# Optimization experiments

Measured on AMD Instinct MI355X. Metric: run time of the kernel, lower is better.

The kernel has to match this reference:

```python
import jax, jax.numpy as jnp
import numpy as np

NUM_HEADS = 16
HEAD_DIM = 64
MEMORY_SIZE = 65536
K_SIMILAR = 8
K_CONTIGUOUS = 2
SURPRISE_THRESHOLD = 0.5
EPS = 1e-8  # torch F.cosine_similarity eps


def setup_inputs() -> dict:
    key = jax.random.key(0)
    ks = jax.random.split(key, 6)
    B, H, S, HD = 4, NUM_HEADS, 8192, HEAD_DIM
    D = H * HD
    inputs = jax.random.normal(ks[0], (B, S, D), dtype=jnp.float32)
    q = jax.random.normal(ks[1], (B, H, S, HD), dtype=jnp.float32)
    k = jax.random.normal(ks[2], (B, H, S, HD), dtype=jnp.float32)
    v = jax.random.normal(ks[3], (B, H, S, HD), dtype=jnp.float32)
    attention_mask = jnp.ones((B, S), dtype=jnp.float32)
    events = jax.random.normal(ks[4], (MEMORY_SIZE, D), dtype=jnp.float32)
    return {"inputs": inputs, "q": q, "k": k, "v": v,
            "attention_mask": attention_mask, "events": events,
            "seq_len_q": 8192}


def _segment_mean(kf, seg, S):
    # kf: [S, D], seg: [S] int32 segment ids (exclusive cumsum of boundary mask)
    sums = jax.ops.segment_sum(kf, seg, num_segments=S)          # [S, D]
    cnts = jax.ops.segment_sum(jnp.ones_like(seg, jnp.float32), seg, num_segments=S)
    means = sums / jnp.maximum(cnts, 1.0)[:, None]
    return means, cnts


def reference(inputs, q, k, v, attention_mask, events, seq_len_q):
    B, H, S, HD = k.shape
    D = H * HD
    # flatten keys per token: [B, S, H*HD]
    kf = k.transpose(0, 2, 1, 3).reshape(B, S, D)

    # --- surprise scores: ||k_t - k_{t-1}|| padded with 0 at t=0 ---
    diffs = kf[:, 1:] - kf[:, :-1]
    norms = jnp.linalg.norm(diffs, axis=-1)                      # [B, S-1]
    surprise = jnp.pad(norms, ((0, 0), (1, 0)))                  # [B, S]

    # --- event segmentation (threshold = mean + c*std, unbiased std like torch) ---
    mean = jnp.mean(surprise, axis=1, keepdims=True)
    std = jnp.std(surprise, axis=1, ddof=1, keepdims=True)
    bmask = surprise > (mean + SURPRISE_THRESHOLD * std)
    bmask = bmask.at[:, -1].set(True)                            # last index is always a boundary
    bi = bmask.astype(jnp.int32)
    seg = jnp.cumsum(bi, axis=1) - bi                            # token t -> #boundaries before t

    # --- memory update: mean-pool keys within each event (scatter) ---
    new_events, event_lengths = jax.vmap(_segment_mean, in_axes=(0, 0, None))(kf, seg, S)
    # new_events: [B, S, D] (rows >= num_events are zero), event_lengths: [B, S]

    # --- retrieval: cosine sim of last-token key vs memory, top-k gather ---
    query = kf[:, -1]                                            # [B, D]
    qn = jnp.maximum(jnp.linalg.norm(query, axis=-1), EPS)       # [B]
    en = jnp.maximum(jnp.linalg.norm(events, axis=-1), EPS)      # [M]
    sims = (query @ events.T) / (qn[:, None] * en[None, :])      # [B, M]
    kt = min(K_SIMILAR + K_CONTIGUOUS, events.shape[0])
    _, idx = jax.lax.top_k(sims, kt)                             # [B, kt]

    ret = events[idx]                                            # [B, kt, D]
    ret = ret.reshape(B, kt, H, HD).transpose(0, 2, 1, 3)        # [B, H, kt, HD]
    ret_k, ret_v = ret, ret                                      # non-differential: v == k slice

    aug_k = jnp.concatenate([ret_k, k], axis=2)                  # [B, H, kt+S, HD]
    aug_v = jnp.concatenate([ret_v, v], axis=2)
    aug_mask = jnp.concatenate([jnp.ones((B, kt), attention_mask.dtype), attention_mask], axis=1)

    cp = seq_len_q - 1
    ret_pos = jnp.linspace(float(cp - kt), float(cp - 1), kt, dtype=jnp.float32)
    pos = jnp.arange(S, dtype=jnp.float32)
    aug_positions = jnp.broadcast_to(jnp.concatenate([ret_pos, pos]), (B, kt + S))

    return (inputs, q, aug_k, aug_v, aug_mask, aug_positions, new_events, event_lengths)
```

## Files before the change

kernel.cpp:

```cpp
#include <hip/hip_runtime.h>
#include <math.h>

#define BB 4
#define HH 16
#define SS 8192
#define HDD 64
#define DD 1024
#define MEM 65536
#define KT 10
#define AUGROWS (SS + KT)

static const long O0 = 0;
static const long O1 = 33554432;
static const long O2 = 67108864;
static const long O3 = 100704256;
static const long O4 = 134299648;
static const long O5 = 134332456;
static const long O6 = 134365264;
static const long O7 = 167919696;

#define WS_NEED_FUSED 5767168UL

#define N4REG 8388608L

typedef float __attribute__((ext_vector_type(4))) f4v;

static __device__ __forceinline__ void nt_store4(float4* p, float4 v) {
    f4v t; t.x = v.x; t.y = v.y; t.z = v.z; t.w = v.w;
    __builtin_nontemporal_store(t, (f4v*)p);
}
static __device__ __forceinline__ float4 nt_load4(const float4* p) {
    f4v t = __builtin_nontemporal_load((const f4v*)p);
    float4 v; v.x = t.x; v.y = t.y; v.z = t.z; v.w = t.w;
    return v;
}

#define K_BLOCKS 2048
#define SIMS_BLOCKS 4096
__global__ __launch_bounds__(256) void bigfused_kernel(
        const float4* __restrict__ k4, const float4* __restrict__ events4,
        float4* __restrict__ out4, double* __restrict__ partial,
        float* __restrict__ sims, int do_part) {
    __shared__ float4 qls4[BB][256];
    int blk = blockIdx.x;
    int tid = threadIdx.x;
    if (blk < K_BLOCKS) {
        long i = ((long)blk) * 256 + tid;
        const long bstride = (long)K_BLOCKS * 256;
        for (; i < N4REG; i += bstride) {
            long chunk = i >> 17;
            long r = i & 131071;
            float4 cur = k4[i];
            out4[(O2 >> 2) + chunk * 131232L + 160 + r] = cur;
            if (do_part) {
                int s = (int)(r >> 4);
                if (s > 0) {
                    float4 pv = k4[i - 16];
                    double dx = (double)cur.x - (double)pv.x;
                    double dy = (double)cur.y - (double)pv.y;
                    double dz = (double)cur.z - (double)pv.z;
                    double dw = (double)cur.w - (double)pv.w;
                    double acc = dx * dx + dy * dy + dz * dz + dw * dw;
                    acc += __shfl_xor(acc, 1, 64);
                    acc += __shfl_xor(acc, 2, 64);
                    acc += __shfl_xor(acc, 4, 64);
                    acc += __shfl_xor(acc, 8, 64);
                    if ((tid & 15) == 0) {
                        int b = (int)(chunk >> 4);
                        int h = (int)(chunk & 15);
                        partial[((long)b * SS + s) * HH + h] = acc;
                    }
                }
            }
        }
    } else {
        for (int j = tid; j < BB * 256; j += 256) {
            int b = j >> 8;
            int f4i = j & 255;
            qls4[b][f4i] =
                k4[((long)(b * HH + (f4i >> 4)) * SS + (SS - 1)) * 16 + (f4i & 15)];
        }
        __syncthreads();
        int w = tid >> 6;
        int lane = tid & 63;
        long e0 = (long)(blk - K_BLOCKS) * 4 + w;
        for (int rr = 0; rr < 4; ++rr) {
            long e = e0 + (long)rr * (4 * SIMS_BLOCKS);
            const float4* er = events4 + e * 256;
            float en = 0.f, d0 = 0.f, d1 = 0.f, d2 = 0.f, d3 = 0.f;
#pragma unroll
            for (int it = 0; it < 4; ++it) {
                int j4 = lane + it * 64;
                float4 ev = nt_load4(er + j4);
                en += ev.x * ev.x + ev.y * ev.y + ev.z * ev.z + ev.w * ev.w;
                float4 q0 = qls4[0][j4];
                d0 += ev.x * q0.x + ev.y * q0.y + ev.z * q0.z + ev.w * q0.w;
                float4 q1 = qls4[1][j4];
                d1 += ev.x * q1.x + ev.y * q1.y + ev.z * q1.z + ev.w * q1.w;
                float4 q2 = qls4[2][j4];
                d2 += ev.x * q2.x + ev.y * q2.y + ev.z * q2.z + ev.w * q2.w;
                float4 q3 = qls4[3][j4];
                d3 += ev.x * q3.x + ev.y * q3.y + ev.z * q3.z + ev.w * q3.w;
            }
            for (int m = 32; m >= 1; m >>= 1) {
                en += __shfl_xor(en, m, 64);
                d0 += __shfl_xor(d0, m, 64);
                d1 += __shfl_xor(d1, m, 64);
                d2 += __shfl_xor(d2, m, 64);
                d3 += __shfl_xor(d3, m, 64);
            }
            if (lane == 0) {
                float enn = fmaxf(sqrtf(en), 1e-8f);
                sims[0 * (long)MEM + e] = d0 / enn;
                sims[1 * (long)MEM + e] = d1 / enn;
                sims[2 * (long)MEM + e] = d2 / enn;
                sims[3 * (long)MEM + e] = d3 / enn;
            }
        }
    }
}

__global__ __launch_bounds__(256) void surprise_fallback_kernel(
        const float* __restrict__ k, double* __restrict__ surprise) {
    int wid = (int)(((long)blockIdx.x * blockDim.x + threadIdx.x) >> 6);
    int lane = threadIdx.x & 63;
    if (wid >= BB * SS) return;
    int b = wid >> 13;
    int s = wid & (SS - 1);
    double acc = 0.0;
    if (s > 0) {
        const float* kb = k + (long)b * HH * SS * HDD;
        for (int h = 0; h < HH; ++h) {
            long off = ((long)h * SS + s) * HDD + lane;
            double d = (double)kb[off] - (double)kb[off - HDD];
            acc += d * d;
        }
        for (int m = 32; m >= 1; m >>= 1) acc += __shfl_xor(acc, m, 64);
    }
    if (lane == 0) surprise[wid] = (s == 0) ? 0.0 : sqrt(acc);
}

__global__ __launch_bounds__(1024) void postfused_kernel(
        const double* __restrict__ partial, double* __restrict__ surprise,
        int* __restrict__ bpos, int* __restrict__ nseg,
        const float* __restrict__ sims, float* __restrict__ cval,
        int* __restrict__ cidx, int* __restrict__ idxout,
        const float* __restrict__ amask, const void* __restrict__ seqp,
        float* __restrict__ out, int* __restrict__ counters, int fused) {
    __shared__ double sd[1024];
    __shared__ int si[1024];
    __shared__ float lv[256][KT];
    __shared__ int li[256][KT];
    int blk = blockIdx.x;
    int tid = threadIdx.x;

    if (blk < 32) {
        if (fused) {
            int t = blk * 1024 + tid;
            int s = t & (SS - 1);
            double acc = 0.0;
            if (s > 0) {
                const double* row = partial + (long)t * HH;
#pragma unroll
                for (int h = 0; h < HH; ++h) acc += row[h];
            }
            surprise[t] = (s == 0) ? 0.0 : sqrt(acc);
        }
        __threadfence();
        __syncthreads();
        if (tid == 0) atomicAdd(&counters[0], 1);
    } else if (blk < 36) {
        if (tid == 0) {
            while (atomicAdd(&counters[0], 0) < 32) __builtin_amdgcn_s_sleep(8);
        }
        __syncthreads();
        __threadfence();
        int b = blk - 32;
        const double* sp = surprise + (long)b * SS;
        double loc[8];
        double sum = 0.0;
        for (int j = 0; j < 8; ++j) { loc[j] = sp[tid * 8 + j]; sum += loc[j]; }
        sd[tid] = sum;
        __syncthreads();
        for (int off = 512; off >= 1; off >>= 1) {
            if (tid < off) sd[tid] += sd[tid + off];
            __syncthreads();
        }
        double mean = sd[0] / SS;
        __syncthreads();
        double vs = 0.0;
        for (int j = 0; j < 8; ++j) { double d = loc[j] - mean; vs += d * d; }
        sd[tid] = vs;
        __syncthreads();
        for (int off = 512; off >= 1; off >>= 1) {
            if (tid < off) sd[tid] += sd[tid + off];
            __syncthreads();
        }
        double thr = mean + 0.5 * sqrt(sd[0] / (SS - 1));
        __syncthreads();
        int bi[8];
        int cnt = 0;
        for (int j = 0; j < 8; ++j) {
            int s = tid * 8 + j;
            bi[j] = (s == SS - 1) || (loc[j] > thr);
            cnt += bi[j];
        }
        si[tid] = cnt;
        __syncthreads();
        for (int off = 1; off < 1024; off <<= 1) {
            int v = 0;
            if (tid >= off) v = si[tid - off];
            __syncthreads();
            si[tid] += v;
            __syncthreads();
        }
        int run = si[tid] - cnt;
        for (int j = 0; j < 8; ++j) {
            if (bi[j]) { bpos[(long)b * SS + run] = tid * 8 + j; ++run; }
        }
        if (tid == 1023) nseg[b] = si[1023];
    } else if (blk < 100) {
        int g = blk - 36;
        int b = g >> 4;
        int part = g & 15;
        if (tid < 256) {
            const float* sb = sims + (long)b * MEM + part * 4096;
            float val[KT];
            int idx[KT];
#pragma unroll
            for (int p = 0; p < KT; ++p) { val[p] = -INFINITY; idx[p] = 0x7fffffff; }
            for (int it = 0; it < 16; ++it) {
                int e = tid + it * 256;
                float v = sb[e];
                if (v > val[KT - 1]) {
#pragma unroll
                    for (int p = KT - 1; p >= 1; --p) {
                        if (v > val[p - 1]) {
                            val[p] = val[p - 1];
                            idx[p] = idx[p - 1];
                        } else {
                            val[p] = v;
                            idx[p] = e;
                            v = -INFINITY;
                        }
                    }
                    if (v != -INFINITY) { val[0] = v; idx[0] = e; }
                }
            }
#pragma unroll
            for (int p = 0; p < KT; ++p) { lv[tid][p] = val[p]; li[tid][p] = idx[p]; }
        }
        for (int off = 128; off >= 1; off >>= 1) {
            __syncthreads();
            if (tid < off) {
                float a_[KT], b_[KT], m_[KT];
                int ai_[KT], bi_[KT], mi_[KT];
#pragma unroll
                for (int p = 0; p < KT; ++p) {
                    a_[p] = lv[tid][p];
                    ai_[p] = li[tid][p];
                    b_[p] = lv[tid + off][p];
                    bi_[p] = li[tid + off][p];
                }
                int pa = 0, pb = 0;
#pragma unroll
                for (int p = 0; p < KT; ++p) {
                    bool ta = (a_[pa] > b_[pb]) ||
                              (a_[pa] == b_[pb] && ai_[pa] < bi_[pb]);
                    if (ta) { m_[p] = a_[pa]; mi_[p] = ai_[pa]; ++pa; }
                    else    { m_[p] = b_[pb]; mi_[p] = bi_[pb]; ++pb; }
                }
#pragma unroll
                for (int p = 0; p < KT; ++p) { lv[tid][p] = m_[p]; li[tid][p] = mi_[p]; }
            }
        }
        __syncthreads();
        if (tid == 0) {
#pragma unroll
            for (int p = 0; p < KT; ++p) {
                cval[g * KT + p] = lv[0][p];
                cidx[g * KT + p] = part * 4096 + li[0][p];
            }
        }
        __threadfence();
        __syncthreads();
        if (tid == 0) atomicAdd(&counters[1], 1);
    } else if (blk < 104) {
        if (tid == 0) {
            while (atomicAdd(&counters[1], 0) < 64) __builtin_amdgcn_s_sleep(8);
        }
        __syncthreads();
        __threadfence();
        int b = blk - 100;
        float mv = -INFINITY;
        int mi = 0x7fffffff;
        if (tid < 160) { mv = cval[b * 160 + tid]; mi = cidx[b * 160 + tid]; }
        if (tid < 256) { lv[tid][0] = mv; li[tid][0] = mi; }
        __syncthreads();
        if (tid == 0) {
            for (int p = 0; p < KT; ++p) {
                float best = -INFINITY;
                int bi = 0x7fffffff;
                int bslot = 0;
                for (int j = 0; j < 160; ++j) {
                    if (lv[j][0] > best || (lv[j][0] == best && li[j][0] < bi)) {
                        best = lv[j][0];
                        bi = li[j][0];
                        bslot = j;
                    }
                }
                idxout[b * KT + p] = bi;
                lv[bslot][0] = -INFINITY;
                li[bslot][0] = 0x7fffffff;
            }
        }
    } else {
        int iv = ((const int*)seqp)[0];
        int seqlen;
        if (iv > 0 && iv < (1 << 24)) seqlen = iv;
        else seqlen = (int)(((const float*)seqp)[0]);
        int cp = seqlen - 1;
        int n = BB * AUGROWS;
        int i = (blk - 104) * 1024 + tid;
        int stride = 16 * 1024;
        for (; i < n; i += stride) {
            int b = i / AUGROWS;
            int t = i - b * AUGROWS;
            out[O4 + i] = (t < KT) ? 1.0f : amask[(long)b * SS + t - KT];
            out[O5 + i] = (t < KT) ? (float)(cp - KT + t) : (float)(t - KT);
        }
    }
}

__global__ __launch_bounds__(256) void segtail_kernel(
        const float4* __restrict__ out4c, const int* __restrict__ bpos,
        const int* __restrict__ nseg, const float* __restrict__ events,
        const int* __restrict__ idxin, float* __restrict__ out) {
    int blk = blockIdx.x;
    int tid = threadIdx.x;
    float4* ne4 = (float4*)(out + O6);
    if (blk < BB * SS) {
        int b = blk >> 13;
        int j = blk & (SS - 1);
        int ns = nseg[b];
        float4* row = ne4 + ((long)b * SS + j) * 256;
        if (j >= ns) {
            nt_store4(row + tid, make_float4(0.f, 0.f, 0.f, 0.f));
            if (tid == 0) out[O7 + (long)b * SS + j] = 0.0f;
            return;
        }
        int start = (j == 0) ? 0 : bpos[(long)b * SS + j - 1] + 1;
        int end = bpos[(long)b * SS + j];
        const float4* kb = out4c + (O2 >> 2) +
                           ((long)(b * HH + (tid >> 4)) * AUGROWS + KT) * 16 +
                           (tid & 15);
        double a0 = 0.0, a1 = 0.0, a2 = 0.0, a3 = 0.0;
        for (int s = start; s <= end; ++s) {
            float4 x = kb[(long)s * 16];
            a0 += (double)x.x; a1 += (double)x.y; a2 += (double)x.z; a3 += (double)x.w;
        }
        double inv = 1.0 / (double)(end - start + 1);
        nt_store4(row + tid, make_float4((float)(a0 * inv), (float)(a1 * inv),
                                         (float)(a2 * inv), (float)(a3 * inv)));
        if (tid == 0) out[O7 + (long)b * SS + j] = (float)(end - start + 1);
    } else {
        int g = blk - BB * SS;
        int b = g / KT;
        int t = g % KT;
        int ev = idxin[b * KT + t];
        for (int c = 0; c < 4; ++c) {
            int j = tid + c * 256;
            float vv = events[(long)ev * DD + j];
            int h = j >> 6;
            int d = j & 63;
            long dst = (((long)b * HH + h) * AUGROWS + t) * HDD + d;
            out[O2 + dst] = vv;
            out[O3 + dst] = vv;
        }
    }
}

extern "C" void kernel_launch(void* const* d_in, const int* in_sizes, int n_in,
                              void* d_out, int out_size, void* d_ws, size_t ws_size,
                              hipStream_t stream) {
    const float* in_inputs = (const float*)d_in[0];
    const float* in_q = (const float*)d_in[1];
    const float* in_k = (const float*)d_in[2];
    const float* in_v = (const float*)d_in[3];
    const float* in_amask = (const float*)d_in[4];
    const float* in_events = (const float*)d_in[5];
    const void* in_seq = d_in[6];
    float* out = (float*)d_out;

    char* ws = (char*)d_ws;
    double* surprise = (double*)ws;
    float* sims = (float*)(ws + 262144);
    int* bpos = (int*)(ws + 1310720);
    int* nseg = (int*)(ws + 1441792);
    int* idxw = (int*)(ws + 1441824);
    float* cval = (float*)(ws + 1442304);
    int* cidx = (int*)(ws + 1444864);
    int* counters = (int*)(ws + 1447424);
    double* partial = (double*)(ws + 1572864);

    const int fused = (ws_size >= WS_NEED_FUSED) ? 1 : 0;

    hipMemsetAsync(counters, 0, 64, stream);
    hipMemcpyAsync(out + O0, in_inputs, 134217728, hipMemcpyDeviceToDevice,
                   stream);
    hipMemcpyAsync(out + O1, in_q, 134217728, hipMemcpyDeviceToDevice, stream);
    hipMemcpy2DAsync(out + O3 + (long)KT * HDD, (size_t)AUGROWS * HDD * 4,
                     in_v, (size_t)SS * HDD * 4, (size_t)SS * HDD * 4,
                     (size_t)BB * HH, hipMemcpyDeviceToDevice, stream);
    bigfused_kernel<<<K_BLOCKS + SIMS_BLOCKS, 256, 0, stream>>>(
        (const float4*)in_k, (const float4*)in_events, (float4*)out, partial,
        sims, fused);
    if (!fused)
        surprise_fallback_kernel<<<8192, 256, 0, stream>>>(in_k, surprise);
    postfused_kernel<<<120, 1024, 0, stream>>>(
        partial, surprise, bpos, nseg, sims, cval, cidx, idxw, in_amask,
        in_seq, out, counters, fused);
    segtail_kernel<<<BB * SS + BB * KT, 256, 0, stream>>>(
        (const float4*)out, bpos, nseg, in_events, idxw, out);
}
```

Measured before the change: 473.7 us.

## Replace hipMemcpy copies with one fused grid-stride copy kernel; split sims kernel

The three runtime memcpy calls (inputs, q, strided v) are dropped. All four tensor copies (inputs, q, k, v), plus the surprise partials computed from k, now run in a single grid-stride kernel that uses nontemporal loads and stores. The cosine-similarity part that used to share a kernel with the k copy becomes its own kernel and launches first. This removes runtime copy overhead and the serialization between copies, but the sims work no longer overlaps with the k copy inside one launch.

```diff
diff --git a/kernel.cpp b/kernel.cpp
--- a/kernel.cpp
+++ b/kernel.cpp
@@ -35,27 +35,34 @@
     return v;
 }
 
-#define K_BLOCKS 2048
-#define SIMS_BLOCKS 4096
-__global__ __launch_bounds__(256) void bigfused_kernel(
-        const float4* __restrict__ k4, const float4* __restrict__ events4,
-        float4* __restrict__ out4, double* __restrict__ partial,
-        float* __restrict__ sims, int do_part) {
-    __shared__ float4 qls4[BB][256];
-    int blk = blockIdx.x;
-    int tid = threadIdx.x;
-    if (blk < K_BLOCKS) {
-        long i = ((long)blk) * 256 + tid;
-        const long bstride = (long)K_BLOCKS * 256;
-        for (; i < N4REG; i += bstride) {
-            long chunk = i >> 17;
-            long r = i & 131071;
-            float4 cur = k4[i];
+#define CPY_BLOCKS 4096
+__global__ __launch_bounds__(256) void copyall_kernel(
+        const float4* __restrict__ in0, const float4* __restrict__ q,
+        const float4* __restrict__ k4, const float4* __restrict__ v,
+        float4* __restrict__ out4, double* __restrict__ partial, int do_part) {
+    long gtid = (long)blockIdx.x * 256 + threadIdx.x;
+    const long stride = (long)CPY_BLOCKS * 256;
+    for (long i = gtid; i < 4 * N4REG; i += stride) {
+        int region = (int)(i >> 23);
+        long rel = i & (N4REG - 1);
+        if (region == 0) {
+            nt_store4(out4 + (O0 >> 2) + rel, nt_load4(in0 + rel));
+        } else if (region == 1) {
+            nt_store4(out4 + (O1 >> 2) + rel, nt_load4(q + rel));
+        } else if (region == 3) {
+            long chunk = rel >> 17;
+            long r = rel & 131071;
+            nt_store4(out4 + (O3 >> 2) + chunk * 131232L + 160 + r,
+                      nt_load4(v + rel));
+        } else {
+            long chunk = rel >> 17;
+            long r = rel & 131071;
+            float4 cur = k4[rel];
             out4[(O2 >> 2) + chunk * 131232L + 160 + r] = cur;
             if (do_part) {
                 int s = (int)(r >> 4);
                 if (s > 0) {
-                    float4 pv = k4[i - 16];
+                    float4 pv = k4[rel - 16];
                     double dx = (double)cur.x - (double)pv.x;
                     double dy = (double)cur.y - (double)pv.y;
                     double dz = (double)cur.z - (double)pv.z;
@@ -65,7 +72,7 @@
                     acc += __shfl_xor(acc, 2, 64);
                     acc += __shfl_xor(acc, 4, 64);
                     acc += __shfl_xor(acc, 8, 64);
-                    if ((tid & 15) == 0) {
+                    if ((threadIdx.x & 15) == 0) {
                         int b = (int)(chunk >> 4);
                         int h = (int)(chunk & 15);
                         partial[((long)b * SS + s) * HH + h] = acc;
@@ -73,49 +80,57 @@
                 }
             }
         }
-    } else {
-        for (int j = tid; j < BB * 256; j += 256) {
-            int b = j >> 8;
-            int f4i = j & 255;
-            qls4[b][f4i] =
-                k4[((long)(b * HH + (f4i >> 4)) * SS + (SS - 1)) * 16 + (f4i & 15)];
-        }
-        __syncthreads();
-        int w = tid >> 6;
-        int lane = tid & 63;
-        long e0 = (long)(blk - K_BLOCKS) * 4 + w;
-        for (int rr = 0; rr < 4; ++rr) {
-            long e = e0 + (long)rr * (4 * SIMS_BLOCKS);
-            const float4* er = events4 + e * 256;
-            float en = 0.f, d0 = 0.f, d1 = 0.f, d2 = 0.f, d3 = 0.f;
-#pragma unroll
-            for (int it = 0; it < 4; ++it) {
-                int j4 = lane + it * 64;
-                float4 ev = nt_load4(er + j4);
-                en += ev.x * ev.x + ev.y * ev.y + ev.z * ev.z + ev.w * ev.w;
-                float4 q0 = qls4[0][j4];
-                d0 += ev.x * q0.x + ev.y * q0.y + ev.z * q0.z + ev.w * q0.w;
-                float4 q1 = qls4[1][j4];
-                d1 += ev.x * q1.x + ev.y * q1.y + ev.z * q1.z + ev.w * q1.w;
-                float4 q2 = qls4[2][j4];
-                d2 += ev.x * q2.x + ev.y * q2.y + ev.z * q2.z + ev.w * q2.w;
-                float4 q3 = qls4[3][j4];
-                d3 += ev.x * q3.x + ev.y * q3.y + ev.z * q3.z + ev.w * q3.w;
-            }
-            for (int m = 32; m >= 1; m >>= 1) {
-                en += __shfl_xor(en, m, 64);
-                d0 += __shfl_xor(d0, m, 64);
-                d1 += __shfl_xor(d1, m, 64);
-                d2 += __shfl_xor(d2, m, 64);
-                d3 += __shfl_xor(d3, m, 64);
-            }
-            if (lane == 0) {
-                float enn = fmaxf(sqrtf(en), 1e-8f);
-                sims[0 * (long)MEM + e] = d0 / enn;
-                sims[1 * (long)MEM + e] = d1 / enn;
-                sims[2 * (long)MEM + e] = d2 / enn;
-                sims[3 * (long)MEM + e] = d3 / enn;
-            }
+    }
+}
+
+#define SIMS_BLOCKS 4096
+__global__ __launch_bounds__(256) void sims_kernel(
+        const float4* __restrict__ k4, const float4* __restrict__ events4,
+        float* __restrict__ sims) {
+    __shared__ float4 qls4[BB][256];
+    int blk = blockIdx.x;
+    int tid = threadIdx.x;
+    for (int j = tid; j < BB * 256; j += 256) {
+        int b = j >> 8;
+        int f4i = j & 255;
+        qls4[b][f4i] =
+            k4[((long)(b * HH + (f4i >> 4)) * SS + (SS - 1)) * 16 + (f4i & 15)];
+    }
+    __syncthreads();
+    int w = tid >> 6;
+    int lane = tid & 63;
+    long e0 = (long)blk * 4 + w;
+    for (int rr = 0; rr < 4; ++rr) {
+        long e = e0 + (long)rr * (4 * SIMS_BLOCKS);
+        const float4* er = events4 + e * 256;
+        float en = 0.f, d0 = 0.f, d1 = 0.f, d2 = 0.f, d3 = 0.f;
+#pragma unroll
+        for (int it = 0; it < 4; ++it) {
+            int j4 = lane + it * 64;
+            float4 ev = nt_load4(er + j4);
+            en += ev.x * ev.x + ev.y * ev.y + ev.z * ev.z + ev.w * ev.w;
+            float4 q0 = qls4[0][j4];
+            d0 += ev.x * q0.x + ev.y * q0.y + ev.z * q0.z + ev.w * q0.w;
+            float4 q1 = qls4[1][j4];
+            d1 += ev.x * q1.x + ev.y * q1.y + ev.z * q1.z + ev.w * q1.w;
+            float4 q2 = qls4[2][j4];
+            d2 += ev.x * q2.x + ev.y * q2.y + ev.z * q2.z + ev.w * q2.w;
+            float4 q3 = qls4[3][j4];
+            d3 += ev.x * q3.x + ev.y * q3.y + ev.z * q3.z + ev.w * q3.w;
+        }
+        for (int m = 32; m >= 1; m >>= 1) {
+            en += __shfl_xor(en, m, 64);
+            d0 += __shfl_xor(d0, m, 64);
+            d1 += __shfl_xor(d1, m, 64);
+            d2 += __shfl_xor(d2, m, 64);
+            d3 += __shfl_xor(d3, m, 64);
+        }
+        if (lane == 0) {
+            float enn = fmaxf(sqrtf(en), 1e-8f);
+            sims[0 * (long)MEM + e] = d0 / enn;
+            sims[1 * (long)MEM + e] = d1 / enn;
+            sims[2 * (long)MEM + e] = d2 / enn;
+            sims[3 * (long)MEM + e] = d3 / enn;
         }
     }
 }
@@ -406,15 +421,11 @@
     const int fused = (ws_size >= WS_NEED_FUSED) ? 1 : 0;
 
     hipMemsetAsync(counters, 0, 64, stream);
-    hipMemcpyAsync(out + O0, in_inputs, 134217728, hipMemcpyDeviceToDevice,
-                   stream);
-    hipMemcpyAsync(out + O1, in_q, 134217728, hipMemcpyDeviceToDevice, stream);
-    hipMemcpy2DAsync(out + O3 + (long)KT * HDD, (size_t)AUGROWS * HDD * 4,
-                     in_v, (size_t)SS * HDD * 4, (size_t)SS * HDD * 4,
-                     (size_t)BB * HH, hipMemcpyDeviceToDevice, stream);
-    bigfused_kernel<<<K_BLOCKS + SIMS_BLOCKS, 256, 0, stream>>>(
-        (const float4*)in_k, (const float4*)in_events, (float4*)out, partial,
-        sims, fused);
+    sims_kernel<<<SIMS_BLOCKS, 256, 0, stream>>>(
+        (const float4*)in_k, (const float4*)in_events, sims);
+    copyall_kernel<<<CPY_BLOCKS, 256, 0, stream>>>(
+        (const float4*)in_inputs, (const float4*)in_q, (const float4*)in_k,
+        (const float4*)in_v, (float4*)out, partial, fused);
     if (!fused)
         surprise_fallback_kernel<<<8192, 256, 0, stream>>>(in_k, surprise);
     postfused_kernel<<<120, 1024, 0, stream>>>(
```

Measured after the change: 439.6 us. 7.2% less time.
